# Performance work log

Hardware: AMD Instinct MI355X
Metric: run time of the kernel (lower is better)

## Reference

```python
import jax, jax.numpy as jnp
import numpy as np

D_MODEL = 768
NUM_HEADS = 12
D_K = D_MODEL // NUM_HEADS


def setup_inputs() -> dict:
    key = jax.random.key(0)
    ks = jax.random.split(key, 11)
    B, S = 2, 2048
    scale = 1.0 / np.sqrt(D_MODEL)
    inp = {
        'query': jax.random.normal(ks[0], (B, S, D_MODEL), jnp.float32),
        'key': jax.random.normal(ks[1], (B, S, D_MODEL), jnp.float32),
        'value': jax.random.normal(ks[2], (B, S, D_MODEL), jnp.float32),
        # Linear params (torch nn.Linear: y = x @ W.T + b); store as [in,out]
        'Wq': jax.random.normal(ks[3], (D_MODEL, D_MODEL), jnp.float32) * scale,
        'bq': jnp.zeros((D_MODEL,), jnp.float32),
        'Wk': jax.random.normal(ks[4], (D_MODEL, D_MODEL), jnp.float32) * scale,
        'bk': jnp.zeros((D_MODEL,), jnp.float32),
        'Wv': jax.random.normal(ks[5], (D_MODEL, D_MODEL), jnp.float32) * scale,
        'bv': jnp.zeros((D_MODEL,), jnp.float32),
        'Wo': jax.random.normal(ks[6], (D_MODEL, D_MODEL), jnp.float32) * scale,
        'bo': jnp.zeros((D_MODEL,), jnp.float32),
    }
    return inp


def _split_heads(x):
    B, S, _ = x.shape
    return x.reshape(B, S, NUM_HEADS, D_K).transpose(0, 2, 1, 3)  # [B,H,S,d_k]


def reference(query, key, value, Wq, bq, Wk, bk, Wv, bv, Wo, bo):
    q = _split_heads(query @ Wq + bq)
    k = _split_heads(key @ Wk + bk)
    v = _split_heads(value @ Wv + bv)
    scores = jnp.einsum('bhqd,bhkd->bhqk', q, k) / np.sqrt(D_K)  # [B,H,S,S]
    attn = jax.nn.softmax(scores, axis=-1)
    x = jnp.einsum('bhqk,bhkd->bhqd', attn, v)  # [B,H,S,d_k]
    B, H, S, _ = x.shape
    x = x.transpose(0, 2, 1, 3).reshape(B, S, D_MODEL)
    return x @ Wo + bo
```

## Files before the change

### kernel.cpp

```cpp
#include <hip/hip_runtime.h>
#include <hip/hip_bf16.h>

#define DM     768
#define HEADS  12
#define DK     64
#define SQ     2048
#define BATCH  2
#define ROWS   4096
#define KTILES 24

typedef __attribute__((ext_vector_type(4))) float f32x4;
typedef __bf16 bf16x8 __attribute__((ext_vector_type(8)));
typedef unsigned short u16x8 __attribute__((ext_vector_type(8)));

#define QSCALE 0.180336880f

static __device__ __forceinline__ unsigned short f2bf(float f) {
    union { float f; unsigned u; } v; v.f = f;
    unsigned u = v.u;
    unsigned lsb = (u >> 16) & 1u;
    u += 0x7fffu + lsb;
    return (unsigned short)(u >> 16);
}

static __device__ __forceinline__ unsigned pack_bf16(float a, float b) {
    __hip_bfloat162 h = __float22bfloat162_rn(make_float2(a, b));
    unsigned u;
    __builtin_memcpy(&u, &h, 4);
    return u;
}

static __device__ __forceinline__ bf16x8 load_bf16x8(const unsigned short* p) {
    u16x8 u = *(const u16x8*)p;
    return __builtin_bit_cast(bf16x8, u);
}

static __device__ __forceinline__ void gld_lds16(const unsigned short* g, unsigned short* l) {
    __builtin_amdgcn_global_load_lds((const __attribute__((address_space(1))) void*)g,
                                     (__attribute__((address_space(3))) void*)l,
                                     16, 0, 0);
}

static __device__ __forceinline__ void drain_dma() {
    asm volatile("s_waitcnt vmcnt(0)" ::: "memory");
}

__global__ __launch_bounds__(256) void cvt_frag3(const float* __restrict__ X0,
                                                 const float* __restrict__ X1,
                                                 const float* __restrict__ X2,
                                                 unsigned short* __restrict__ A0,
                                                 unsigned short* __restrict__ A1,
                                                 unsigned short* __restrict__ A2) {
    int z = blockIdx.z;
    const float* X = z == 0 ? X0 : z == 1 ? X1 : X2;
    unsigned short* A = z == 0 ? A0 : z == 1 ? A1 : A2;
    int p = blockIdx.x * 256 + threadIdx.x;
    int lane = p & 63;
    int g = p >> 6;
    int ks = g % KTILES;
    int mt = g / KTILES;
    int row = mt * 16 + (lane & 15);
    int k   = ks * 32 + (lane >> 4) * 8;
    const float* src = X + (size_t)row * DM + k;
    float4 v0 = *(const float4*)src;
    float4 v1 = *(const float4*)(src + 4);
    u16x8 o;
    o[0]=f2bf(v0.x); o[1]=f2bf(v0.y); o[2]=f2bf(v0.z); o[3]=f2bf(v0.w);
    o[4]=f2bf(v1.x); o[5]=f2bf(v1.y); o[6]=f2bf(v1.z); o[7]=f2bf(v1.w);
    *(u16x8*)(A + (size_t)p * 8) = o;
}

__global__ __launch_bounds__(256) void wt_frag4(const float* __restrict__ W0,
                                                const float* __restrict__ W1,
                                                const float* __restrict__ W2,
                                                const float* __restrict__ W3,
                                                unsigned short* __restrict__ F0,
                                                unsigned short* __restrict__ F1,
                                                unsigned short* __restrict__ F2,
                                                unsigned short* __restrict__ F3) {
    int z = blockIdx.z;
    const float* W = z == 0 ? W0 : z == 1 ? W1 : z == 2 ? W2 : W3;
    unsigned short* F = z == 0 ? F0 : z == 1 ? F1 : z == 2 ? F2 : F3;
    int p = blockIdx.x * 256 + threadIdx.x;
    int lane = p & 63;
    int t = (p >> 6) & 3;
    int g = p >> 8;
    int ks = g % KTILES;
    int nb = g / KTILES;
    int n = nb * 64 + t * 16 + (lane & 15);
    int k = ks * 32 + (lane >> 4) * 8;
    u16x8 o;
#pragma unroll
    for (int j = 0; j < 8; ++j) o[j] = f2bf(W[(size_t)(k + j) * DM + n]);
    *(u16x8*)(F + (size_t)p * 8) = o;
}

__global__ __launch_bounds__(256) void gemm_qkv(const unsigned short* __restrict__ A0,
                                                const unsigned short* __restrict__ A1,
                                                const unsigned short* __restrict__ A2,
                                                const unsigned short* __restrict__ F0,
                                                const unsigned short* __restrict__ F1,
                                                const unsigned short* __restrict__ F2,
                                                const float* __restrict__ b0,
                                                const float* __restrict__ b1,
                                                const float* __restrict__ b2,
                                                unsigned short* __restrict__ Qo,
                                                unsigned short* __restrict__ Ko,
                                                unsigned short* __restrict__ Vo) {
    __shared__ __align__(16) unsigned short ldsB[2][8192];

    int z = blockIdx.z;
    const unsigned short* A = z == 0 ? A0 : z == 1 ? A1 : A2;
    const unsigned short* F = z == 0 ? F0 : z == 1 ? F1 : F2;
    const float* bias        = z == 0 ? b0 : z == 1 ? b1 : b2;

    int w    = threadIdx.x >> 6;
    int lane = threadIdx.x & 63;
    int l15  = lane & 15;
    int quad = lane >> 4;
    int m0 = blockIdx.y * 128 + w * 32;
    int nb = blockIdx.x;
    int mt0 = m0 >> 4;

    const unsigned short* Ap = A + (size_t)mt0 * KTILES * 512 + lane * 8;
    const unsigned short* Bsrc = F + (size_t)nb * KTILES * 4 * 512 + w * 2048 + lane * 8;
    unsigned short* Bdst = &ldsB[0][w * 2048];

    f32x4 acc[2][4];
#pragma unroll
    for (int i = 0; i < 2; ++i)
#pragma unroll
        for (int t = 0; t < 4; ++t) acc[i][t] = (f32x4){0.f, 0.f, 0.f, 0.f};

#define BSTAGE(buf, c) do { \
        _Pragma("unroll") \
        for (int j = 0; j < 4; ++j) \
            gld_lds16(Bsrc + (size_t)(c) * 8192 + j * 512, Bdst + (buf) * 8192 + j * 512); \
    } while (0)

    BSTAGE(0, 0);

    for (int c = 0; c < 6; ++c) {
        drain_dma();
        __syncthreads();
        if (c < 5) BSTAGE((c + 1) & 1, c + 1);
        const unsigned short* Bl = &ldsB[c & 1][0];
#pragma unroll
        for (int k4 = 0; k4 < 4; ++k4) {
            bf16x8 a[2];
#pragma unroll
            for (int i = 0; i < 2; ++i)
                a[i] = load_bf16x8(Ap + ((size_t)i * KTILES + c * 4 + k4) * 512);
#pragma unroll
            for (int t = 0; t < 4; ++t) {
                bf16x8 bb = load_bf16x8(Bl + (k4 * 4 + t) * 512 + lane * 8);
#pragma unroll
                for (int i = 0; i < 2; ++i)
                    acc[i][t] = __builtin_amdgcn_mfma_f32_16x16x32_bf16(a[i], bb, acc[i][t], 0, 0, 0);
            }
        }
    }
#undef BSTAGE

    float scale = (z == 0) ? QSCALE : 1.0f;
#pragma unroll
    for (int t = 0; t < 4; ++t) {
        int col = nb * 64 + t * 16 + l15;
        float bv = bias[col];
        int h = col >> 6, d = col & (DK - 1);
#pragma unroll
        for (int i = 0; i < 2; ++i)
#pragma unroll
            for (int r = 0; r < 4; ++r) {
                int row = m0 + i * 16 + quad * 4 + r;
                float v = (acc[i][t][r] + bv) * scale;
                int bb = row >> 11, s = row & (SQ - 1);
                size_t bh = (size_t)(bb * HEADS + h);
                if (z == 0) {
                    Qo[(bh * SQ + s) * DK + d] = f2bf(v);
                } else if (z == 1) {
                    int sc = s & 63;
                    Ko[(bh * (SQ / 64) + (s >> 6)) * 4096 + sc * 64 +
                       (((d >> 3) ^ ((sc >> 1) & 7)) << 3) + (d & 7)] = f2bf(v);
                } else {
                    int sc = s & 63;
                    Vo[(bh * (SQ / 64) + (s >> 6)) * 4096 + d * 64 +
                       (((sc >> 3) ^ ((d >> 1) & 7)) << 3) + (sc & 7)] = f2bf(v);
                }
            }
    }
}

__global__ __launch_bounds__(256) void flash_attn(const unsigned short* __restrict__ Q,
                                                  const unsigned short* __restrict__ Kb,
                                                  const unsigned short* __restrict__ Vb,
                                                  unsigned short* __restrict__ Af) {
    __shared__ __align__(16) unsigned short ldsK[2][4096];
    __shared__ __align__(16) unsigned short ldsV[2][4096];
    __shared__ __align__(16) unsigned short ldsP[4][32 * 72];

    int w    = threadIdx.x >> 6;
    int lane = threadIdx.x & 63;
    int l15  = lane & 15;
    int quad = lane >> 4;
    int rg   = w >> 1;
    int par  = w & 1;
    int b = blockIdx.z, h = blockIdx.y;
    int q0 = blockIdx.x * 64 + rg * 32;

    size_t bh = (size_t)(b * HEADS + h);
    const unsigned short* Qp = Q  + (bh * SQ + q0) * DK;
    const unsigned short* KB = Kb + bh * (SQ / 64) * 4096;
    const unsigned short* VB = Vb + bh * (SQ / 64) * 4096;

    bf16x8 aq[2][2];
#pragma unroll
    for (int i = 0; i < 2; ++i) {
        aq[i][0] = load_bf16x8(Qp + (i * 16 + l15) * DK + quad * 8);
        aq[i][1] = load_bf16x8(Qp + (i * 16 + l15) * DK + 32 + quad * 8);
    }

    f32x4 o[2][4];
#pragma unroll
    for (int i = 0; i < 2; ++i)
#pragma unroll
        for (int t = 0; t < 4; ++t) o[i][t] = (f32x4){0.f, 0.f, 0.f, 0.f};
    float lsum[2][4] = {{0.f,0.f,0.f,0.f},{0.f,0.f,0.f,0.f}};

    unsigned short* Pw = &ldsP[w][0];

    int koff[4][2], voff[4][2];
#pragma unroll
    for (int t = 0; t < 4; ++t) {
        int pr = (t >> 1) * 32 + 2 * l15 + (t & 1);
        int sw = l15 & 7;
        koff[t][0] = pr * 64 + (((quad)     ^ sw) << 3);
        koff[t][1] = pr * 64 + (((4 + quad) ^ sw) << 3);
        int d = t * 16 + l15;
        int swv = (l15 >> 1) & 7;
        voff[t][0] = d * 64 + (((quad)     ^ swv) << 3);
        voff[t][1] = d * 64 + (((4 + quad) ^ swv) << 3);
    }

    const unsigned short* ksrc = KB + rg * 2048 + lane * 8;
    const unsigned short* vsrc = VB + rg * 2048 + lane * 8;
    unsigned short* kdst = &ldsK[par][rg * 2048];
    unsigned short* vdst = &ldsV[par][rg * 2048];

#define STAGE(n) do { \
        _Pragma("unroll") \
        for (int j = 0; j < 4; ++j) { \
            gld_lds16(ksrc + (size_t)(n) * 4096 + j * 512, kdst + j * 512); \
            gld_lds16(vsrc + (size_t)(n) * 4096 + j * 512, vdst + j * 512); \
        } \
    } while (0)

    STAGE(par);

    const unsigned short* Kl = &ldsK[par][0];
    const unsigned short* Vl = &ldsV[par][0];

    for (int s = 0; s < 16; ++s) {
        drain_dma();
        __syncthreads();

        f32x4 sc[2][4];
#pragma unroll
        for (int i = 0; i < 2; ++i)
#pragma unroll
            for (int t = 0; t < 4; ++t) sc[i][t] = (f32x4){0.f, 0.f, 0.f, 0.f};

#pragma unroll
        for (int t = 0; t < 4; ++t) {
            bf16x8 k0 = load_bf16x8(Kl + koff[t][0]);
            bf16x8 k1 = load_bf16x8(Kl + koff[t][1]);
#pragma unroll
            for (int i = 0; i < 2; ++i) {
                sc[i][t] = __builtin_amdgcn_mfma_f32_16x16x32_bf16(aq[i][0], k0, sc[i][t], 0, 0, 0);
                sc[i][t] = __builtin_amdgcn_mfma_f32_16x16x32_bf16(aq[i][1], k1, sc[i][t], 0, 0, 0);
            }
        }

#pragma unroll
        for (int i = 0; i < 2; ++i)
#pragma unroll
            for (int sub = 0; sub < 2; ++sub)
#pragma unroll
                for (int r = 0; r < 4; ++r) {
                    float e0 = exp2f(sc[i][2 * sub][r]);
                    float e1 = exp2f(sc[i][2 * sub + 1][r]);
                    lsum[i][r] += e0 + e1;
                    *(unsigned*)(Pw + (i * 16 + quad * 4 + r) * 72 + sub * 32 + l15 * 2)
                        = pack_bf16(e0, e1);
                }

        bf16x8 pf[2][2];
#pragma unroll
        for (int i = 0; i < 2; ++i) {
            pf[i][0] = load_bf16x8(Pw + (i * 16 + l15) * 72 + quad * 8);
            pf[i][1] = load_bf16x8(Pw + (i * 16 + l15) * 72 + 32 + quad * 8);
        }

#pragma unroll
        for (int t = 0; t < 4; ++t) {
            bf16x8 v0 = load_bf16x8(Vl + voff[t][0]);
            bf16x8 v1 = load_bf16x8(Vl + voff[t][1]);
#pragma unroll
            for (int i = 0; i < 2; ++i) {
                o[i][t] = __builtin_amdgcn_mfma_f32_16x16x32_bf16(pf[i][0], v0, o[i][t], 0, 0, 0);
                o[i][t] = __builtin_amdgcn_mfma_f32_16x16x32_bf16(pf[i][1], v1, o[i][t], 0, 0, 0);
            }
        }

        __syncthreads();
        if (s < 15) STAGE(2 * s + 2 + par);
    }
#undef STAGE

    float* fO = (float*)&ldsK[0][0];
    float* fL = (float*)&ldsV[0][0];
    if (par == 1) {
#pragma unroll
        for (int i = 0; i < 2; ++i)
#pragma unroll
            for (int r = 0; r < 4; ++r) {
                int rowin = i * 16 + quad * 4 + r;
#pragma unroll
                for (int t = 0; t < 4; ++t)
                    fO[rg * 2048 + rowin * 64 + t * 16 + l15] = o[i][t][r];
                fL[rg * 512 + rowin * 16 + l15] = lsum[i][r];
            }
    }
    __syncthreads();
    if (par == 0) {
#pragma unroll
        for (int i = 0; i < 2; ++i)
#pragma unroll
            for (int r = 0; r < 4; ++r) {
                int rowin = i * 16 + quad * 4 + r;
                float l = lsum[i][r] + fL[rg * 512 + rowin * 16 + l15];
                l += __shfl_xor(l, 1);
                l += __shfl_xor(l, 2);
                l += __shfl_xor(l, 4);
                l += __shfl_xor(l, 8);
                float inv = 1.0f / l;
                int R  = b * SQ + q0 + rowin;
                int mt = R >> 4;
#pragma unroll
                for (int t = 0; t < 4; ++t) {
                    float val = o[i][t][r] + fO[rg * 2048 + rowin * 64 + t * 16 + l15];
                    int ks    = h * 2 + (t >> 1);
                    int quadp = ((t & 1) << 1) + (l15 >> 3);
                    int j     = l15 & 7;
                    Af[(size_t)(mt * KTILES + ks) * 512 +
                       (size_t)((quadp << 4) + (rowin & 15)) * 8 + j] = f2bf(val * inv);
                }
            }
    }
}

__global__ __launch_bounds__(256) void gemm_out(const unsigned short* __restrict__ Af,
                                                const unsigned short* __restrict__ Ff,
                                                const float* __restrict__ bias,
                                                float* __restrict__ out) {
    __shared__ __align__(16) unsigned short ldsB[2][8192];

    int w    = threadIdx.x >> 6;
    int lane = threadIdx.x & 63;
    int l15  = lane & 15;
    int quad = lane >> 4;
    int m0 = blockIdx.y * 64 + w * 16;
    int nb = blockIdx.x;
    int mt = m0 >> 4;

    const unsigned short* Ap = Af + (size_t)mt * KTILES * 512 + lane * 8;
    const unsigned short* Bsrc = Ff + (size_t)nb * KTILES * 4 * 512 + w * 2048 + lane * 8;
    unsigned short* Bdst = &ldsB[0][w * 2048];

    f32x4 acc[4];
#pragma unroll
    for (int t = 0; t < 4; ++t) acc[t] = (f32x4){0.f, 0.f, 0.f, 0.f};

#define BSTAGE(buf, c) do { \
        _Pragma("unroll") \
        for (int j = 0; j < 4; ++j) \
            gld_lds16(Bsrc + (size_t)(c) * 8192 + j * 512, Bdst + (buf) * 8192 + j * 512); \
    } while (0)

    BSTAGE(0, 0);

    for (int c = 0; c < 6; ++c) {
        drain_dma();
        __syncthreads();
        if (c < 5) BSTAGE((c + 1) & 1, c + 1);
        const unsigned short* Bl = &ldsB[c & 1][0];
#pragma unroll
        for (int k4 = 0; k4 < 4; ++k4) {
            bf16x8 a = load_bf16x8(Ap + (size_t)(c * 4 + k4) * 512);
#pragma unroll
            for (int t = 0; t < 4; ++t) {
                bf16x8 bb = load_bf16x8(Bl + (k4 * 4 + t) * 512 + lane * 8);
                acc[t] = __builtin_amdgcn_mfma_f32_16x16x32_bf16(a, bb, acc[t], 0, 0, 0);
            }
        }
    }
#undef BSTAGE

#pragma unroll
    for (int t = 0; t < 4; ++t) {
        int col = nb * 64 + t * 16 + l15;
        float bv = bias[col];
#pragma unroll
        for (int r = 0; r < 4; ++r) {
            int row = m0 + quad * 4 + r;
            out[(size_t)row * DM + col] = acc[t][r] + bv;
        }
    }
}

extern "C" void kernel_launch(void* const* d_in, const int* in_sizes, int n_in,
                              void* d_out, int out_size, void* d_ws, size_t ws_size,
                              hipStream_t stream) {
    const float* query = (const float*)d_in[0];
    const float* key   = (const float*)d_in[1];
    const float* value = (const float*)d_in[2];
    const float* Wq = (const float*)d_in[3];  const float* bq = (const float*)d_in[4];
    const float* Wk = (const float*)d_in[5];  const float* bk = (const float*)d_in[6];
    const float* Wv = (const float*)d_in[7];  const float* bv = (const float*)d_in[8];
    const float* Wo = (const float*)d_in[9];  const float* bo = (const float*)d_in[10];

    const size_t NX = (size_t)ROWS * DM;
    const size_t NW = (size_t)DM * DM;
    unsigned short* Xq  = (unsigned short*)d_ws;
    unsigned short* Xk  = Xq  + NX;
    unsigned short* Xv  = Xk  + NX;
    unsigned short* Qb  = Xv  + NX;
    unsigned short* Kb  = Qb  + NX;
    unsigned short* Vt  = Kb  + NX;
    unsigned short* Wtq = Vt  + NX;
    unsigned short* Wtk = Wtq + NW;
    unsigned short* Wtv = Wtk + NW;
    unsigned short* Wto = Wtv + NW;

    cvt_frag3<<<dim3((unsigned)(NX / 8 / 256), 1, 3), 256, 0, stream>>>(
        query, key, value, Xq, Xk, Xv);

    wt_frag4<<<dim3((unsigned)(NW / 8 / 256), 1, 4), 256, 0, stream>>>(
        Wq, Wk, Wv, Wo, Wtq, Wtk, Wtv, Wto);

    gemm_qkv<<<dim3(DM / 64, ROWS / 128, 3), 256, 0, stream>>>(
        Xq, Xk, Xv, Wtq, Wtk, Wtv, bq, bk, bv, Qb, Kb, Vt);

    flash_attn<<<dim3(SQ / 64, HEADS, BATCH), 256, 0, stream>>>(Qb, Kb, Vt, Xq);

    gemm_out<<<dim3(DM / 64, ROWS / 64), 256, 0, stream>>>(Xq, Wto, bo, (float*)d_out);
}
```

Before: 207.1 us.

## Prefetch A fragments into registers and stage K/V via registers in attention

Measured after the change: 199.4 us. -3.7%, faster.

```diff
diff --git a/kernel.cpp b/kernel.cpp
--- a/kernel.cpp
+++ b/kernel.cpp
@@ -28,6 +28,14 @@
     unsigned u;
     __builtin_memcpy(&u, &h, 4);
     return u;
+}
+
+static __device__ __forceinline__ float fexp2(float x) {
+#if __has_builtin(__builtin_amdgcn_exp2f)
+    return __builtin_amdgcn_exp2f(x);
+#else
+    return exp2f(x);
+#endif
 }
 
 static __device__ __forceinline__ bf16x8 load_bf16x8(const unsigned short* p) {
@@ -140,6 +148,13 @@
 
     BSTAGE(0, 0);
 
+    bf16x8 a_cur[2][4];
+#pragma unroll
+    for (int k4 = 0; k4 < 4; ++k4)
+#pragma unroll
+        for (int i = 0; i < 2; ++i)
+            a_cur[i][k4] = load_bf16x8(Ap + ((size_t)i * KTILES + k4) * 512);
+
     for (int c = 0; c < 6; ++c) {
         drain_dma();
         __syncthreads();
@@ -147,16 +162,17 @@
         const unsigned short* Bl = &ldsB[c & 1][0];
 #pragma unroll
         for (int k4 = 0; k4 < 4; ++k4) {
-            bf16x8 a[2];
-#pragma unroll
-            for (int i = 0; i < 2; ++i)
-                a[i] = load_bf16x8(Ap + ((size_t)i * KTILES + c * 4 + k4) * 512);
 #pragma unroll
             for (int t = 0; t < 4; ++t) {
                 bf16x8 bb = load_bf16x8(Bl + (k4 * 4 + t) * 512 + lane * 8);
 #pragma unroll
                 for (int i = 0; i < 2; ++i)
-                    acc[i][t] = __builtin_amdgcn_mfma_f32_16x16x32_bf16(a[i], bb, acc[i][t], 0, 0, 0);
+                    acc[i][t] = __builtin_amdgcn_mfma_f32_16x16x32_bf16(a_cur[i][k4], bb, acc[i][t], 0, 0, 0);
+            }
+            if (c < 5) {
+#pragma unroll
+                for (int i = 0; i < 2; ++i)
+                    a_cur[i][k4] = load_bf16x8(Ap + ((size_t)i * KTILES + (c + 1) * 4 + k4) * 512);
             }
         }
     }
@@ -244,25 +260,35 @@
 
     const unsigned short* ksrc = KB + rg * 2048 + lane * 8;
     const unsigned short* vsrc = VB + rg * 2048 + lane * 8;
-    unsigned short* kdst = &ldsK[par][rg * 2048];
-    unsigned short* vdst = &ldsV[par][rg * 2048];
-
-#define STAGE(n) do { \
+    unsigned short* kdst = &ldsK[par][rg * 2048 + lane * 8];
+    unsigned short* vdst = &ldsV[par][rg * 2048 + lane * 8];
+
+    u16x8 kreg[4], vreg[4];
+#define STAGE_LOAD(n) do { \
         _Pragma("unroll") \
         for (int j = 0; j < 4; ++j) { \
-            gld_lds16(ksrc + (size_t)(n) * 4096 + j * 512, kdst + j * 512); \
-            gld_lds16(vsrc + (size_t)(n) * 4096 + j * 512, vdst + j * 512); \
+            kreg[j] = *(const u16x8*)(ksrc + (size_t)(n) * 4096 + j * 512); \
+            vreg[j] = *(const u16x8*)(vsrc + (size_t)(n) * 4096 + j * 512); \
         } \
     } while (0)
-
-    STAGE(par);
+#define STAGE_WRITE() do { \
+        _Pragma("unroll") \
+        for (int j = 0; j < 4; ++j) { \
+            *(u16x8*)(kdst + j * 512) = kreg[j]; \
+            *(u16x8*)(vdst + j * 512) = vreg[j]; \
+        } \
+    } while (0)
+
+    STAGE_LOAD(par);
+    STAGE_WRITE();
 
     const unsigned short* Kl = &ldsK[par][0];
     const unsigned short* Vl = &ldsV[par][0];
 
     for (int s = 0; s < 16; ++s) {
-        drain_dma();
         __syncthreads();
+
+        if (s < 15) STAGE_LOAD(2 * s + 2 + par);
 
         f32x4 sc[2][4];
 #pragma unroll
@@ -287,8 +313,8 @@
             for (int sub = 0; sub < 2; ++sub)
 #pragma unroll
                 for (int r = 0; r < 4; ++r) {
-                    float e0 = exp2f(sc[i][2 * sub][r]);
-                    float e1 = exp2f(sc[i][2 * sub + 1][r]);
+                    float e0 = fexp2(sc[i][2 * sub][r]);
+                    float e1 = fexp2(sc[i][2 * sub + 1][r]);
                     lsum[i][r] += e0 + e1;
                     *(unsigned*)(Pw + (i * 16 + quad * 4 + r) * 72 + sub * 32 + l15 * 2)
                         = pack_bf16(e0, e1);
@@ -313,9 +339,10 @@
         }
 
         __syncthreads();
-        if (s < 15) STAGE(2 * s + 2 + par);
-    }
-#undef STAGE
+        if (s < 15) STAGE_WRITE();
+    }
+#undef STAGE_LOAD
+#undef STAGE_WRITE
 
     float* fO = (float*)&ldsK[0][0];
     float* fL = (float*)&ldsV[0][0];
@@ -389,6 +416,11 @@
 
     BSTAGE(0, 0);
 
+    bf16x8 a_cur[4];
+#pragma unroll
+    for (int k4 = 0; k4 < 4; ++k4)
+        a_cur[k4] = load_bf16x8(Ap + (size_t)k4 * 512);
+
     for (int c = 0; c < 6; ++c) {
         drain_dma();
         __syncthreads();
@@ -396,12 +428,13 @@
         const unsigned short* Bl = &ldsB[c & 1][0];
 #pragma unroll
         for (int k4 = 0; k4 < 4; ++k4) {
-            bf16x8 a = load_bf16x8(Ap + (size_t)(c * 4 + k4) * 512);
 #pragma unroll
             for (int t = 0; t < 4; ++t) {
                 bf16x8 bb = load_bf16x8(Bl + (k4 * 4 + t) * 512 + lane * 8);
-                acc[t] = __builtin_amdgcn_mfma_f32_16x16x32_bf16(a, bb, acc[t], 0, 0, 0);
-            }
+                acc[t] = __builtin_amdgcn_mfma_f32_16x16x32_bf16(a_cur[k4], bb, acc[t], 0, 0, 0);
+            }
+            if (c < 5)
+                a_cur[k4] = load_bf16x8(Ap + (size_t)((c + 1) * 4 + k4) * 512);
         }
     }
 #undef BSTAGE
```
